# Optimization experiments

Hardware: AMD Instinct MI355X
Metric: run time of the kernel (lower is better)

The kernel has to match this reference:

```python
import jax, jax.numpy as jnp
import numpy as np

SL, BS, HS, FFN = 2048, 1, 512, 2048
E, TOP_K = 8, 2


def setup_inputs() -> dict:
    key = jax.random.key(0)
    k_x, k_w, k_i, k_w1, k_w2 = jax.random.split(key, 5)
    x = jax.random.normal(k_x, (SL, BS, HS), dtype=jnp.float32)
    expert_weights = jax.random.uniform(k_w, (SL * BS, TOP_K), dtype=jnp.float32)
    expert_indices = jax.random.randint(k_i, (SL * BS, TOP_K), 0, E, dtype=jnp.int32)
    # grouped expert MLP params (megablocks GroupedMLP, regular type, no bias)
    w1 = jax.random.normal(k_w1, (E, HS, FFN), dtype=jnp.float32) * (HS ** -0.5)
    w2 = jax.random.normal(k_w2, (E, FFN, HS), dtype=jnp.float32) * (FFN ** -0.5)
    return {"x": x, "expert_weights": expert_weights, "expert_indices": expert_indices,
            "w1": w1, "w2": w2}


def reference(x, expert_weights, expert_indices, w1, w2):
    sl, bs, hs = x.shape
    n_tok = sl * bs
    xf = x.reshape(n_tok, hs)                      # [N, hs]
    ew = expert_weights.reshape(-1)                # [N*top_k]
    ei = expert_indices.reshape(-1)                # [N*top_k]

    # indices_and_bins: stable radix sort of assignments by expert id
    indices = jnp.argsort(ei)                      # stable in jax -> sorted assignment ids
    bin_ids = ei[indices]                          # sorted expert id per assignment

    # megablocks gather: row for assignment i is indices[i] // top_k
    rows = indices // TOP_K                        # [T]
    xg = xf[rows]                                  # [T, hs] expert-contiguous tokens

    # grouped GEMM expert MLP (dense masked loop over fixed expert count)
    outg = jnp.zeros_like(xg)
    for e in range(E):
        m = (bin_ids == e).astype(x.dtype)[:, None]
        h = jax.nn.gelu(xg @ w1[e], approximate=False)   # [T, ffn]
        outg = outg + m * (h @ w2[e])                    # [T, hs]

    # buffer.index_add_(0, E*input_indices + bin_ids, output.detach())
    buf_idx = E * rows + bin_ids
    buffer = jnp.zeros((n_tok * E, hs), x.dtype).at[buf_idx].add(
        jax.lax.stop_gradient(outg))

    # megablocks scatter: weighted combine back to token order
    y = jnp.zeros((n_tok, hs), x.dtype).at[rows].add(outg * ew[indices][:, None])
    return y.reshape(sl, bs, hs), buffer.reshape(n_tok, E, hs)
```

## Files before the change

kernel.cpp:

```cpp
#include <hip/hip_runtime.h>
#include <hip/hip_bf16.h>

#define NTOK 2048
#define TOPK 2
#define HS   512
#define FFN  2048
#define NE   8
#define TASSIGN (NTOK*TOPK)
#define PAD  5120
#define MAXT128 40
#define MAXT64  72

typedef __attribute__((ext_vector_type(8))) short bf16x8;
typedef __attribute__((ext_vector_type(8))) unsigned short u16x8;
typedef __attribute__((ext_vector_type(4))) float f32x4;

static const size_t OFF_XBF  = 0;
static const size_t OFF_W1T  = 2097152;
static const size_t OFF_W2T  = 18874368;
static const size_t OFF_H    = 35651584;
static const size_t OFF_OUTV = 56623104;
static const size_t OFF_RT   = 67108864;
static const size_t OFF_HROF = 67129344;
static const size_t OFF_TE128= 67145728;
static const size_t OFF_TR128= 67145888;
static const size_t OFF_TE64 = 67146048;
static const size_t OFF_TR64 = 67146336;

__device__ __forceinline__ unsigned short f2bf(float f) {
    union { __hip_bfloat16 h; unsigned short u; } v;
    v.h = __float2bfloat16(f);
    return v.u;
}

__device__ __forceinline__ float bf2f(unsigned short u) {
    union { unsigned int i; float f; } v;
    v.i = ((unsigned int)u) << 16;
    return v.f;
}

__device__ __forceinline__ int swz(int r, int byte_off) {
    return byte_off ^ ((r & 7) << 4);
}

__device__ __forceinline__ float gelu_fast(float x) {
    float z2 = x * fmaf(0.0713548162726f, x * x, 1.5957691216057f);
    float e = __expf(z2);
    return x - __fdividef(x, e + 1.0f);
}

#define GLOAD16(gsrc, ldst) \
    __builtin_amdgcn_global_load_lds((const __attribute__((address_space(1))) void*)(gsrc), \
                                     (__attribute__((address_space(3))) void*)(ldst), 16, 0, 0)

__device__ __forceinline__ void dev_transpose(const float* __restrict__ in,
                                              unsigned short* __restrict__ out,
                                              int R, int C, int e, int rb, int cb, int tid) {
    __shared__ unsigned short t[32][33];
    int tx = tid & 31, ty = tid >> 5;
    const float* ip = in + (size_t)e * R * C;
    unsigned short* op = out + (size_t)e * C * R;
#pragma unroll
    for (int i = 0; i < 4; i++) {
        int r = ty + i * 8;
        t[r][tx] = f2bf(ip[(size_t)(rb + r) * C + cb + tx]);
    }
    __syncthreads();
#pragma unroll
    for (int i = 0; i < 4; i++) {
        int c = ty + i * 8;
        op[(size_t)(cb + c) * R + rb + tx] = t[tx][c];
    }
}

__global__ __launch_bounds__(256) void k_prep(
        const float* __restrict__ x, const float* __restrict__ w1,
        const float* __restrict__ w2, const int* __restrict__ ei,
        unsigned short* __restrict__ xbf, unsigned short* __restrict__ w1T,
        unsigned short* __restrict__ w2T,
        int* __restrict__ rowtok, int* __restrict__ hrof,
        int* __restrict__ te128, int* __restrict__ tr128,
        int* __restrict__ te64, int* __restrict__ tr64) {
    int b = blockIdx.x;
    int tid = threadIdx.x;
    if (b == 0) {
        __shared__ int cnt[NE], offpad[NE], cur[NE];
        for (int i = tid; i < PAD; i += 256) rowtok[i] = 0;
        if (tid < NE) cnt[tid] = 0;
        __syncthreads();
        for (int a = tid; a < TASSIGN; a += 256) atomicAdd(&cnt[ei[a]], 1);
        __syncthreads();
        if (tid == 0) {
            int o = 0, t1 = 0, t2 = 0;
            for (int e = 0; e < NE; e++) {
                offpad[e] = o; cur[e] = 0;
                for (int r = 0; r < cnt[e]; r += 128) { te128[t1] = e; tr128[t1] = o + r; t1++; }
                for (int r = 0; r < cnt[e]; r += 64)  { te64[t2]  = e; tr64[t2]  = o + r; t2++; }
                o += (cnt[e] + 127) / 128 * 128;
            }
            for (; t1 < MAXT128; t1++) te128[t1] = -1;
            for (; t2 < MAXT64;  t2++) te64[t2]  = -1;
        }
        __syncthreads();
        for (int a = tid; a < TASSIGN; a += 256) {
            int e = ei[a];
            int r = atomicAdd(&cur[e], 1);
            int hr = offpad[e] + r;
            rowtok[hr] = a >> 1;
            hrof[a] = hr;
        }
    } else if (b < 1 + 1024) {
        int i = ((b - 1) * 256 + tid) * 4;
        float4 v = *(const float4*)(x + i);
        ushort4 o;
        o.x = f2bf(v.x); o.y = f2bf(v.y); o.z = f2bf(v.z); o.w = f2bf(v.w);
        *(ushort4*)(xbf + i) = o;
    } else if (b < 1 + 1024 + 8192) {
        int blk = b - 1025;
        int e = blk >> 10, rem = blk & 1023;
        dev_transpose(w1, w1T, HS, FFN, e, (rem >> 6) * 32, (rem & 63) * 32, tid);
    } else {
        int blk = b - 9217;
        int e = blk >> 10, rem = blk & 1023;
        dev_transpose(w2, w2T, FFN, HS, e, (rem >> 4) * 32, (rem & 15) * 32, tid);
    }
}

template<int BM, int BN, int KFULL, int KLOC, bool G1>
__global__ __launch_bounds__(256) void k_gemm(
        const unsigned short* __restrict__ A,
        const unsigned short* __restrict__ B,
        unsigned short* __restrict__ outp,
        const int* __restrict__ rowtok,
        const int* __restrict__ te, const int* __restrict__ tr, int N) {
    constexpr int MI = BM / 32, NJ = BN / 32;
    constexpr int PA = BM / 32, PB = BN / 32;
    constexpr int ABYTES = BM * 64 * 2, BBYTES = BN * 64 * 2;
    constexpr int NSTEP = KLOC / 64;
    static_assert(NSTEP % 2 == 0, "even steps");

    int mt = blockIdx.y;
    int e = te[mt];
    if (e < 0) return;
    int hr0 = tr[mt];
    int ct = blockIdx.x;
    int kz = blockIdx.z;
    int k0 = kz * KLOC;

    __shared__ int4 ldsv[(2 * (ABYTES + BBYTES)) / 16];
    char* A0 = (char*)ldsv;
    char* A1 = A0 + ABYTES;
    char* B0 = A1 + ABYTES;
    char* B1 = B0 + BBYTES;

    int tid = threadIdx.x;
    int lane = tid & 63, wave = tid >> 6;
    int wm = wave >> 1, wn = wave & 1;

    const char* asrc[PA];
    const char* bsrc[PB];
    int adoff[PA], bdoff[PB];
#pragma unroll
    for (int p = 0; p < PA; p++) {
        int idx = p * 256 + tid;
        int r = idx >> 3, c8 = idx & 7;
        int c8s = c8 ^ (r & 7);
        size_t row = G1 ? (size_t)rowtok[hr0 + r] : (size_t)(hr0 + r);
        asrc[p] = (const char*)(A + row * KFULL + k0) + c8s * 16;
        adoff[p] = (p * 256 + wave * 64) * 16;
    }
#pragma unroll
    for (int p = 0; p < PB; p++) {
        int idx = p * 256 + tid;
        int r = idx >> 3, c8 = idx & 7;
        int c8s = c8 ^ (r & 7);
        bsrc[p] = (const char*)(B + ((size_t)e * N + (size_t)ct * BN + r) * KFULL + k0) + c8s * 16;
        bdoff[p] = (p * 256 + wave * 64) * 16;
    }

    f32x4 acc[MI][NJ] = {};

    auto stage = [&](char* Ad, char* Bd, int s) {
        int kb = s * 128;
#pragma unroll
        for (int p = 0; p < PA; p++) GLOAD16(asrc[p] + kb, Ad + adoff[p]);
#pragma unroll
        for (int p = 0; p < PB; p++) GLOAD16(bsrc[p] + kb, Bd + bdoff[p]);
    };
    auto compute = [&](const char* As, const char* Bs) {
#pragma unroll
        for (int kk = 0; kk < 64; kk += 32) {
            bf16x8 af[MI], bfv[NJ];
#pragma unroll
            for (int i = 0; i < MI; i++) {
                int ar = wm * (BM / 2) + i * 16 + (lane & 15);
                af[i] = *(const bf16x8*)(As + swz(ar, ar * 128 + kk * 2 + (lane >> 4) * 16));
            }
#pragma unroll
            for (int j = 0; j < NJ; j++) {
                int bc = wn * (BN / 2) + j * 16 + (lane & 15);
                bfv[j] = *(const bf16x8*)(Bs + swz(bc, bc * 128 + kk * 2 + (lane >> 4) * 16));
            }
#pragma unroll
            for (int i = 0; i < MI; i++)
#pragma unroll
                for (int j = 0; j < NJ; j++)
                    acc[i][j] = __builtin_amdgcn_mfma_f32_16x16x32_bf16(af[i], bfv[j], acc[i][j], 0, 0, 0);
        }
    };

    stage(A0, B0, 0);
    __syncthreads();
#pragma unroll 1
    for (int s = 0; s < NSTEP; s += 2) {
        if (s + 1 < NSTEP) stage(A1, B1, s + 1);
        compute(A0, B0);
        __syncthreads();
        if (s + 2 < NSTEP) stage(A0, B0, s + 2);
        compute(A1, B1);
        __syncthreads();
    }

    if constexpr (G1) {
#pragma unroll
        for (int i = 0; i < MI; i++)
#pragma unroll
            for (int j = 0; j < NJ; j++)
#pragma unroll
                for (int q = 0; q < 4; q++) {
                    int row = hr0 + wm * (BM / 2) + i * 16 + (lane >> 4) * 4 + q;
                    int col = ct * BN + wn * (BN / 2) + j * 16 + (lane & 15);
                    outp[(size_t)row * N + col] = f2bf(gelu_fast(acc[i][j][q]));
                }
    } else {
        unsigned short* O = outp + (size_t)kz * PAD * HS;
#pragma unroll
        for (int i = 0; i < MI; i++)
#pragma unroll
            for (int j = 0; j < NJ; j++)
#pragma unroll
                for (int q = 0; q < 4; q++) {
                    int row = hr0 + wm * (BM / 2) + i * 16 + (lane >> 4) * 4 + q;
                    int col = ct * BN + wn * (BN / 2) + j * 16 + (lane & 15);
                    O[(size_t)row * N + col] = f2bf(acc[i][j][q]);
                }
    }
}

__global__ __launch_bounds__(256) void k_combine(
        const unsigned short* __restrict__ outv, const int* __restrict__ ei,
        const float* __restrict__ ew, const int* __restrict__ hrof,
        float* __restrict__ y, float* __restrict__ buf) {
    constexpr size_t SPLIT = (size_t)PAD * HS;
    int g = blockIdx.x * 256 + threadIdx.x;
    int t = g >> 6, c8 = g & 63;
    int a0 = 2 * t, a1 = a0 + 1;
    int h0 = hrof[a0], h1 = hrof[a1];
    u16x8 q0a = *(const u16x8*)(outv + (size_t)h0 * HS + c8 * 8);
    u16x8 q0b = *(const u16x8*)(outv + SPLIT + (size_t)h0 * HS + c8 * 8);
    u16x8 q1a = *(const u16x8*)(outv + (size_t)h1 * HS + c8 * 8);
    u16x8 q1b = *(const u16x8*)(outv + SPLIT + (size_t)h1 * HS + c8 * 8);
    float w0 = ew[a0], w1 = ew[a1];
    float o0[8], o1[8], yy[8];
#pragma unroll
    for (int k = 0; k < 8; k++) {
        o0[k] = bf2f(q0a[k]) + bf2f(q0b[k]);
        o1[k] = bf2f(q1a[k]) + bf2f(q1b[k]);
        yy[k] = w0 * o0[k] + w1 * o1[k];
    }
    float* yp = y + (size_t)t * HS + c8 * 8;
    *(float4*)(yp)     = make_float4(yy[0], yy[1], yy[2], yy[3]);
    *(float4*)(yp + 4) = make_float4(yy[4], yy[5], yy[6], yy[7]);
    int e0 = ei[a0], e1 = ei[a1];
    float* bt = buf + (size_t)t * (NE * HS) + c8 * 8;
#pragma unroll
    for (int e = 0; e < NE; e++) {
        float v[8];
#pragma unroll
        for (int k = 0; k < 8; k++)
            v[k] = (e == e0 ? o0[k] : 0.0f) + (e == e1 ? o1[k] : 0.0f);
        float* be = bt + (size_t)e * HS;
        *(float4*)(be)     = make_float4(v[0], v[1], v[2], v[3]);
        *(float4*)(be + 4) = make_float4(v[4], v[5], v[6], v[7]);
    }
}

extern "C" void kernel_launch(void* const* d_in, const int* in_sizes, int n_in,
                              void* d_out, int out_size, void* d_ws, size_t ws_size,
                              hipStream_t stream) {
    const float* x  = (const float*)d_in[0];
    const float* ew = (const float*)d_in[1];
    const int*   ei = (const int*)d_in[2];
    const float* w1 = (const float*)d_in[3];
    const float* w2 = (const float*)d_in[4];

    char* ws = (char*)d_ws;
    unsigned short* xbf  = (unsigned short*)(ws + OFF_XBF);
    unsigned short* w1T  = (unsigned short*)(ws + OFF_W1T);
    unsigned short* w2T  = (unsigned short*)(ws + OFF_W2T);
    unsigned short* Hb   = (unsigned short*)(ws + OFF_H);
    unsigned short* outv = (unsigned short*)(ws + OFF_OUTV);
    int*            rowtok = (int*)(ws + OFF_RT);
    int*            hrof   = (int*)(ws + OFF_HROF);
    int*            te128  = (int*)(ws + OFF_TE128);
    int*            tr128  = (int*)(ws + OFF_TR128);
    int*            te64   = (int*)(ws + OFF_TE64);
    int*            tr64   = (int*)(ws + OFF_TR64);

    float* y   = (float*)d_out;
    float* buf = (float*)d_out + (size_t)NTOK * HS;

    k_prep<<<1 + 1024 + 8192 + 8192, 256, 0, stream>>>(
        x, w1, w2, ei, xbf, w1T, w2T, rowtok, hrof, te128, tr128, te64, tr64);
    k_gemm<128, 64, HS, HS, true><<<dim3(FFN / 64, MAXT128), 256, 0, stream>>>(
        xbf, w1T, Hb, rowtok, te128, tr128, FFN);
    k_gemm<64, 64, FFN, FFN / 2, false><<<dim3(HS / 64, MAXT64, 2), 256, 0, stream>>>(
        Hb, w2T, outv, rowtok, te64, tr64, HS);
    k_combine<<<NTOK * HS / 8 / 256, 256, 0, stream>>>(
        outv, ei, ew, hrof, y, buf);
}
```

Baseline: 88.65 us.

## Deepen GEMM LDS pipeline with fine-grained vmcnt waits and raw barriers

Restructures the double-buffered GEMM main loop so two stages are in flight before compute starts. __syncthreads is replaced with explicit s_waitcnt vmcnt(N) and lgkmcnt(0) plus raw s_barrier wrapped in sched barriers, so global loads for the next stage overlap compute on the current one. The waits rely on the stage function issuing exactly PA+PB vector loads directly into LDS. If that assumption is wrong, results can be read before they arrive.

```diff
diff --git a/kernel.cpp b/kernel.cpp
--- a/kernel.cpp
+++ b/kernel.cpp
@@ -137,7 +137,7 @@
     constexpr int PA = BM / 32, PB = BN / 32;
     constexpr int ABYTES = BM * 64 * 2, BBYTES = BN * 64 * 2;
     constexpr int NSTEP = KLOC / 64;
-    static_assert(NSTEP % 2 == 0, "even steps");
+    static_assert(NSTEP % 2 == 0 && NSTEP >= 4, "even steps >= 4");
 
     int mt = blockIdx.y;
     int e = te[mt];
@@ -208,18 +208,37 @@
                     acc[i][j] = __builtin_amdgcn_mfma_f32_16x16x32_bf16(af[i], bfv[j], acc[i][j], 0, 0, 0);
         }
     };
+    auto waitv_lps = [&]() {
+        if constexpr (PA + PB == 6)      { asm volatile("s_waitcnt vmcnt(6)" ::: "memory"); }
+        else if constexpr (PA + PB == 4) { asm volatile("s_waitcnt vmcnt(4)" ::: "memory"); }
+        else                             { asm volatile("s_waitcnt vmcnt(0)" ::: "memory"); }
+    };
+    auto waitv0 = [&]() { asm volatile("s_waitcnt vmcnt(0)" ::: "memory"); };
+    auto waitlgkm = [&]() { asm volatile("s_waitcnt lgkmcnt(0)" ::: "memory"); };
+    auto bar = [&]() {
+        __builtin_amdgcn_sched_barrier(0);
+        __builtin_amdgcn_s_barrier();
+        __builtin_amdgcn_sched_barrier(0);
+        asm volatile("" ::: "memory");
+    };
 
     stage(A0, B0, 0);
-    __syncthreads();
+    stage(A1, B1, 1);
 #pragma unroll 1
-    for (int s = 0; s < NSTEP; s += 2) {
-        if (s + 1 < NSTEP) stage(A1, B1, s + 1);
+    for (int s = 0; s + 2 < NSTEP; s += 2) {
+        waitv_lps(); bar();
         compute(A0, B0);
-        __syncthreads();
-        if (s + 2 < NSTEP) stage(A0, B0, s + 2);
+        waitlgkm(); bar();
+        stage(A0, B0, s + 2);
+        waitv_lps(); bar();
         compute(A1, B1);
-        __syncthreads();
-    }
+        waitlgkm(); bar();
+        if (s + 3 < NSTEP) stage(A1, B1, s + 3);
+    }
+    waitv_lps(); bar();
+    compute(A0, B0);
+    waitv0(); bar();
+    compute(A1, B1);
 
     if constexpr (G1) {
 #pragma unroll
```

Measured after the change: 83.95 us (median of 2 runs). 1.06x faster.
